# Performance work log

Measured on AMD Instinct MI355X. Metric: run time of the kernel, lower is better.

The kernel has to match this reference:

```python
import jax, jax.numpy as jnp
import numpy as np

# --- physics constants (from source) ---
T_STALL = 5.4 * (1.0 / 100.0)
W_FREE = 1620.0 * (1.0 / 60.0) * 2.0 * np.pi
L_X = 0.129907
L_Y = 0.095724
A = L_X + L_Y
R = 4 * 0.0254
MASS = 6.0
INERTIA = MASS
MOMENT_OF_INERTIA = MASS * (12 * 0.0254) ** 2 / 6.0

LV2WV = np.array([[1, -1, -A], [1, 1, A], [1, 1, -A], [1, -1, A]], dtype=np.float32) / R  # [4,3]
CD2MD = np.array([[1, -1, -1], [1, 1, 1], [1, 1, -1], [1, -1, 1]], dtype=np.float32)      # [4,3]
WT2LA = (LV2WV.T / np.array([INERTIA, INERTIA, MOMENT_OF_INERTIA], dtype=np.float32)[:, None]).astype(np.float32)  # [3,4]

BATCH = 4_000_000


def _rot(c, s):
    # builds [..., 3, 3] = [[c,-s,0],[s,c,0],[0,0,1]]
    z = jnp.zeros_like(c)
    o = jnp.ones_like(c)
    return jnp.stack([
        jnp.stack([c, -s, z], axis=-1),
        jnp.stack([s, c, z], axis=-1),
        jnp.stack([z, z, o], axis=-1),
    ], axis=-2)


def setup_inputs() -> dict:
    key = jax.random.key(0)
    k1, k2 = jax.random.split(key)
    state = jax.random.normal(k1, (BATCH, 6), dtype=jnp.float32)
    control_duty = jax.random.normal(k2, (3,), dtype=jnp.float32)
    t = jnp.zeros((1,), dtype=jnp.float32)
    return {"t": t, "state": state, "control_duty": control_duty}


def reference(t, state, control_duty):
    lv2wv = jnp.asarray(LV2WV)
    cd2md = jnp.asarray(CD2MD)
    wt2la = jnp.asarray(WT2LA)

    absolute_vel = state[..., 3:]            # [..., 3]
    theta = state[..., 2]                    # [...]

    # absolute -> local frame
    a2l = _rot(jnp.cos(-theta), jnp.sin(-theta))                      # [...,3,3]
    local_vel = jnp.einsum('...ij,...j->...i', a2l, absolute_vel)     # [...,3]
    wheel_vel = jnp.einsum('ij,...j->...i', lv2wv, local_vel)         # [...,4]

    motor_duty = cd2md @ control_duty                                 # [4]
    is_same_direction = (jnp.sign(motor_duty * wheel_vel) + 1.0) / 2.0
    wheel_torque = T_STALL * (1.0 - jnp.abs(wheel_vel) * is_same_direction / W_FREE) * motor_duty  # [...,4]

    local_accel = jnp.einsum('ij,...j->...i', wt2la, wheel_torque)    # [...,3]

    # local -> absolute frame
    l2a = _rot(jnp.cos(theta), jnp.sin(theta))
    absolute_accel = jnp.einsum('...ij,...j->...i', l2a, local_accel)

    return jnp.concatenate([absolute_vel, absolute_accel], axis=-1)   # [...,6]
```

## Files before the change

kernel.cpp:

```cpp
#include <hip/hip_runtime.h>
#include <math.h>

namespace k {
constexpr double dA     = 0.129907 + 0.095724;
constexpr double dR     = 4.0 * 0.0254;
constexpr double dI     = 6.0;
constexpr double dMOI   = 6.0 * (12.0 * 0.0254) * (12.0 * 0.0254) / 6.0;
constexpr float T_STALL   = (float)(5.4 / 100.0);
constexpr float INV_WFREE = (float)(1.0 / (1620.0 / 60.0 * 2.0 * 3.14159265358979323846));
constexpr float A         = (float)dA;
constexpr float INV_R     = (float)(1.0 / dR);
constexpr float INV_RI    = (float)(1.0 / (dR * dI));
constexpr float A_RMOI    = (float)(dA / (dR * dMOI));
}

__device__ __forceinline__ float wheel_torque(float w, float m) {
    float p = m * w;
    float sgn = (float)(p > 0.0f) - (float)(p < 0.0f);
    float isd = 0.5f * (sgn + 1.0f);
    return k::T_STALL * (1.0f - fabsf(w) * isd * k::INV_WFREE) * m;
}

__device__ __forceinline__ void mecanum_elem(const float st[6],
                                             float m0, float m1, float m2, float m3,
                                             float o[6]) {
    float theta = st[2];
    float s, c;
    sincosf(theta, &s, &c);

    float v0 = st[3], v1 = st[4], v2 = st[5];

    float lv0 = c * v0 + s * v1;
    float lv1 = c * v1 - s * v0;

    float al2 = k::A * v2;
    float w0 = (lv0 - lv1 - al2) * k::INV_R;
    float w1 = (lv0 + lv1 + al2) * k::INV_R;
    float w2 = (lv0 + lv1 - al2) * k::INV_R;
    float w3 = (lv0 - lv1 + al2) * k::INV_R;

    float t0 = wheel_torque(w0, m0);
    float t1 = wheel_torque(w1, m1);
    float t2 = wheel_torque(w2, m2);
    float t3 = wheel_torque(w3, m3);

    float la0 = (t0 + t1 + t2 + t3) * k::INV_RI;
    float la1 = (-t0 + t1 + t2 - t3) * k::INV_RI;
    float la2 = (-t0 + t1 - t2 + t3) * k::A_RMOI;

    float aa0 = c * la0 - s * la1;
    float aa1 = s * la0 + c * la1;

    o[0] = v0; o[1] = v1; o[2] = v2;
    o[3] = aa0; o[4] = aa1; o[5] = la2;
}

#define BLOCK            256
#define WAVES_PER_BLOCK  4
#define PAIRS_PER_WAVE   64
#define F4_PER_WAVE      192

__global__ __launch_bounds__(256) void mecanum_wave_kernel(
    const float4* __restrict__ state4,
    const float* __restrict__ cd,
    float4* __restrict__ out4,
    int n_pairs) {
    __shared__ float4 sbuf[WAVES_PER_BLOCK * F4_PER_WAVE];

    const int tid  = threadIdx.x;
    const int wid  = tid >> 6;
    const int lane = tid & 63;
    float4* ws = sbuf + wid * F4_PER_WAVE;

    const int pair0  = blockIdx.x * BLOCK + wid * PAIRS_PER_WAVE;
    const int f4base = pair0 * 3;
    const int total4 = n_pairs * 3;

    float u0 = cd[0], u1 = cd[1], u2 = cd[2];
    float m0 = u0 - u1 - u2;
    float m1 = u0 + u1 + u2;
    float m2 = u0 + u1 - u2;
    float m3 = u0 - u1 + u2;

#pragma unroll
    for (int j = 0; j < 3; ++j) {
        int g = f4base + j * 64 + lane;
        if (g < total4) ws[j * 64 + lane] = state4[g];
    }

    if (pair0 + lane < n_pairs) {
        float4 a  = ws[3 * lane + 0];
        float4 b  = ws[3 * lane + 1];
        float4 gg = ws[3 * lane + 2];

        float stA[6] = { a.x, a.y, a.z, a.w, b.x, b.y };
        float stB[6] = { b.z, b.w, gg.x, gg.y, gg.z, gg.w };
        float oA[6], oB[6];
        mecanum_elem(stA, m0, m1, m2, m3, oA);
        mecanum_elem(stB, m0, m1, m2, m3, oB);

        ws[3 * lane + 0] = make_float4(oA[0], oA[1], oA[2], oA[3]);
        ws[3 * lane + 1] = make_float4(oA[4], oA[5], oB[0], oB[1]);
        ws[3 * lane + 2] = make_float4(oB[2], oB[3], oB[4], oB[5]);
    }

#pragma unroll
    for (int j = 0; j < 3; ++j) {
        int g = f4base + j * 64 + lane;
        if (g < total4) out4[g] = ws[j * 64 + lane];
    }
}

__global__ void mecanum_tail_kernel(const float* __restrict__ state,
                                    const float* __restrict__ cd,
                                    float* __restrict__ out,
                                    int start, int n) {
    int i = start + blockIdx.x * blockDim.x + threadIdx.x;
    if (i >= n) return;
    float u0 = cd[0], u1 = cd[1], u2 = cd[2];
    float m0 = u0 - u1 - u2;
    float m1 = u0 + u1 + u2;
    float m2 = u0 + u1 - u2;
    float m3 = u0 - u1 + u2;
    float st[6], o[6];
#pragma unroll
    for (int j = 0; j < 6; ++j) st[j] = state[6 * i + j];
    mecanum_elem(st, m0, m1, m2, m3, o);
#pragma unroll
    for (int j = 0; j < 6; ++j) out[6 * i + j] = o[j];
}

extern "C" void kernel_launch(void* const* d_in, const int* in_sizes, int n_in,
                              void* d_out, int out_size, void* d_ws, size_t ws_size,
                              hipStream_t stream) {
    const float* state = (const float*)d_in[1];
    const float* cd    = (const float*)d_in[2];
    float* out         = (float*)d_out;

    int n = in_sizes[1] / 6;
    int n_pairs = n / 2;

    if (n_pairs > 0) {
        int grid = (n_pairs + BLOCK - 1) / BLOCK;
        mecanum_wave_kernel<<<grid, BLOCK, 0, stream>>>(
            (const float4*)state, cd, (float4*)out, n_pairs);
    }
    if (n & 1) {
        mecanum_tail_kernel<<<1, 64, 0, stream>>>(state, cd, out, 2 * n_pairs, n);
    }
}
```

Before: 175.2 us.

## Use persistent grid-stride waves with register prefetch of next tile

Replaces the one-tile-per-wave launch with a capped persistent grid of 1536 blocks where each wave loops over tiles. While it works on the current tile it loads the next tile into registers, so global loads overlap compute and stores. It also stages through LDS with wave barriers instead of relying on implicit ordering. The cost is fewer resident waves per CU for the memory system to hide latency with, and more register use.

```diff
diff --git a/kernel.cpp b/kernel.cpp
--- a/kernel.cpp
+++ b/kernel.cpp
@@ -55,46 +55,66 @@
     o[3] = aa0; o[4] = aa1; o[5] = la2;
 }
 
-#define BLOCK            256
-#define WAVES_PER_BLOCK  4
-#define PAIRS_PER_WAVE   64
-#define F4_PER_WAVE      192
+#define BLOCK           256
+#define WAVES_PER_BLOCK 4
+#define F4_PER_TILE     192
+#define GRID_BLOCKS     1536
 
-__global__ __launch_bounds__(256) void mecanum_wave_kernel(
+__global__ __launch_bounds__(256) void mecanum_stream_kernel(
     const float4* __restrict__ state4,
     const float* __restrict__ cd,
     float4* __restrict__ out4,
     int n_pairs) {
-    __shared__ float4 sbuf[WAVES_PER_BLOCK * F4_PER_WAVE];
+    __shared__ float4 sbuf[WAVES_PER_BLOCK * F4_PER_TILE];
 
     const int tid  = threadIdx.x;
     const int wid  = tid >> 6;
     const int lane = tid & 63;
-    float4* ws = sbuf + wid * F4_PER_WAVE;
+    float4* ws = sbuf + wid * F4_PER_TILE;
 
-    const int pair0  = blockIdx.x * BLOCK + wid * PAIRS_PER_WAVE;
-    const int f4base = pair0 * 3;
-    const int total4 = n_pairs * 3;
+    const int n_tiles = (n_pairs + 63) >> 6;
+    const int total4  = n_pairs * 3;
+    const int stride  = gridDim.x * WAVES_PER_BLOCK;
 
     float u0 = cd[0], u1 = cd[1], u2 = cd[2];
-    float m0 = u0 - u1 - u2;
-    float m1 = u0 + u1 + u2;
-    float m2 = u0 + u1 - u2;
-    float m3 = u0 - u1 + u2;
+    const float m0 = u0 - u1 - u2;
+    const float m1 = u0 + u1 + u2;
+    const float m2 = u0 + u1 - u2;
+    const float m3 = u0 - u1 + u2;
 
-#pragma unroll
-    for (int j = 0; j < 3; ++j) {
-        int g = f4base + j * 64 + lane;
-        if (g < total4) ws[j * 64 + lane] = state4[g];
+    int tile = blockIdx.x * WAVES_PER_BLOCK + wid;
+    if (tile >= n_tiles) return;
+
+    float4 c0 = {0,0,0,0}, c1 = {0,0,0,0}, c2 = {0,0,0,0};
+    {
+        int fb = tile * F4_PER_TILE;
+        if (fb + lane       < total4) c0 = state4[fb + lane];
+        if (fb + 64 + lane  < total4) c1 = state4[fb + 64 + lane];
+        if (fb + 128 + lane < total4) c2 = state4[fb + 128 + lane];
     }
 
-    if (pair0 + lane < n_pairs) {
+    for (; tile < n_tiles; tile += stride) {
+        float4 n0 = {0,0,0,0}, n1 = {0,0,0,0}, n2 = {0,0,0,0};
+        const int next = tile + stride;
+        if (next < n_tiles) {
+            int nb = next * F4_PER_TILE;
+            if (nb + lane       < total4) n0 = state4[nb + lane];
+            if (nb + 64 + lane  < total4) n1 = state4[nb + 64 + lane];
+            if (nb + 128 + lane < total4) n2 = state4[nb + 128 + lane];
+        }
+
+        ws[lane]       = c0;
+        ws[64 + lane]  = c1;
+        ws[128 + lane] = c2;
+        __builtin_amdgcn_wave_barrier();
+
         float4 a  = ws[3 * lane + 0];
         float4 b  = ws[3 * lane + 1];
-        float4 gg = ws[3 * lane + 2];
+        float4 g4 = ws[3 * lane + 2];
+        __builtin_amdgcn_wave_barrier();
 
         float stA[6] = { a.x, a.y, a.z, a.w, b.x, b.y };
-        float stB[6] = { b.z, b.w, gg.x, gg.y, gg.z, gg.w };
+        float stB[6] = { b.z, b.w, g4.x, g4.y, g4.z, g4.w };
         float oA[6], oB[6];
         mecanum_elem(stA, m0, m1, m2, m3, oA);
         mecanum_elem(stB, m0, m1, m2, m3, oB);
@@ -102,12 +122,19 @@
         ws[3 * lane + 0] = make_float4(oA[0], oA[1], oA[2], oA[3]);
         ws[3 * lane + 1] = make_float4(oA[4], oA[5], oB[0], oB[1]);
         ws[3 * lane + 2] = make_float4(oB[2], oB[3], oB[4], oB[5]);
-    }
+        __builtin_amdgcn_wave_barrier();
 
-#pragma unroll
-    for (int j = 0; j < 3; ++j) {
-        int g = f4base + j * 64 + lane;
-        if (g < total4) out4[g] = ws[j * 64 + lane];
+        float4 o0 = ws[lane];
+        float4 o1 = ws[64 + lane];
+        float4 o2 = ws[128 + lane];
+        __builtin_amdgcn_wave_barrier();
+
+        const int fb = tile * F4_PER_TILE;
+        if (fb + lane       < total4) out4[fb + lane]       = o0;
+        if (fb + 64 + lane  < total4) out4[fb + 64 + lane]  = o1;
+        if (fb + 128 + lane < total4) out4[fb + 128 + lane] = o2;
+
+        c0 = n0; c1 = n1; c2 = n2;
     }
 }
 
@@ -141,8 +168,10 @@
     int n_pairs = n / 2;
 
     if (n_pairs > 0) {
-        int grid = (n_pairs + BLOCK - 1) / BLOCK;
-        mecanum_wave_kernel<<<grid, BLOCK, 0, stream>>>(
+        int n_tiles = (n_pairs + 63) >> 6;
+        int need_blocks = (n_tiles + WAVES_PER_BLOCK - 1) / WAVES_PER_BLOCK;
+        int grid = need_blocks < GRID_BLOCKS ? need_blocks : GRID_BLOCKS;
+        mecanum_stream_kernel<<<grid, BLOCK, 0, stream>>>(
             (const float4*)state, cd, (float4*)out, n_pairs);
     }
     if (n & 1) {
```

Result: no change. 176.1 us (+0.5%).
